# Kernel optimization log

Measured on AMD Instinct MI355X. Metric: run time of the kernel, lower is better.

Reference implementation:

```python
import jax, jax.numpy as jnp
import numpy as np

# Structural constants (CSG module-level globals)
S, N = 250, 200            # sequences, peds per sequence (uniform for vectorization)
MAX = 16                   # MAX_CONSIDERED_PED
H, E = 64, 64              # h_dim, EMBEDDING_DIM
HID, BN = 512, 32          # mlp_pre_pool hidden, BOTTLENECK_DIM


def setup_inputs() -> dict:
    key = jax.random.key(0)
    ks = jax.random.split(key, 8)
    g = lambda k, shape, s=0.05: jax.random.normal(k, shape, dtype=jnp.float32) * s
    h_states = jax.random.normal(ks[0], (S * N, H), dtype=jnp.float32)
    last_pos = jax.random.normal(ks[1], (S * N, 2), dtype=jnp.float32) * 5.0
    starts = np.arange(S, dtype=np.int64) * N
    seq_start_end = jnp.asarray(np.stack([starts, starts + N], axis=1))
    return {
        "h_states": h_states,
        "last_pos": last_pos,
        "W_pos": g(ks[2], (2, E)), "b_pos": jnp.zeros((E,), jnp.float32),
        "W1": g(ks[3], (H + E, HID)), "b1": jnp.zeros((HID,), jnp.float32),
        "W2": g(ks[4], (HID, BN)), "b2": jnp.zeros((BN,), jnp.float32),
        "W_attn": g(ks[5], (MAX * BN, MAX)), "b_attn": jnp.zeros((MAX,), jnp.float32),
        "seq_start_end": seq_start_end,
        "train_or_test": 0,
    }


def reference(h_states, last_pos, W_pos, b_pos, W1, b1, W2, b2, W_attn, b_attn,
              seq_start_end, train_or_test):
    h = h_states.reshape(S, N, H)          # per-sequence hidden states
    pos = last_pos.reshape(S, N, 2)
    # social_features[s, i, j] = pos[s, j] - pos[s, i]
    rel = pos[:, None, :, :] - pos[:, :, None, :]          # [S, N, N, 2]
    # pairwise distances only feed argsort -> stop_gradient (avoids sqrt(0) NaN in vjp)
    dist = jnp.linalg.norm(jax.lax.stop_gradient(rel), axis=-1)  # [S, N, N]
    idx = jnp.argsort(dist, axis=-1)
    # original torch code sorts rows by the attached idx-value column then truncates:
    # this selects rows j with idx[s,i,j] < MAX, i.e. the inverse permutation prefix
    sel = jnp.argsort(idx, axis=-1)[..., :MAX]             # [S, N, MAX]
    # gather neighbor hidden states and relative positions
    h_sel = jax.vmap(lambda hh, ss: hh[ss])(h, sel)        # [S, N, MAX, H]
    feat_sel = jnp.take_along_axis(rel, sel[..., None], axis=2)  # [S, N, MAX, 2]
    emb = feat_sel @ W_pos + b_pos                         # pos_embedding, [S,N,MAX,E]
    x = jnp.concatenate([h_sel, emb], axis=-1)             # [S, N, MAX, H+E]
    # mlp_pre_pool: Linear->ReLU, Linear->ReLU (batch_norm off, dropout 0)
    x = jax.nn.relu(x @ W1 + b1)                           # [S, N, MAX, HID]
    x = jax.nn.relu(x @ W2 + b2)                           # [S, N, MAX, BN]
    logits = x.reshape(S, N, MAX * BN) @ W_attn + b_attn   # [S, N, MAX]
    w = jax.nn.softmax(logits, axis=-1)
    out = jnp.sum(x * w[..., None], axis=2)                # attention-weighted pool
    return out.reshape(S * N, BN)
```

## Files before the change

kernel.cpp:

```cpp
#include <hip/hip_runtime.h>
#include <hip/hip_bf16.h>

#define S_CNT 250
#define N_PED 200
#define MAXP  16
#define HID   512
#define BN    32

#define WS1_FRAGS 8192
#define WS2_FRAGS 2048
#define WAF_FRAGS 1024
#define WS_NEED   180224u

typedef __attribute__((ext_vector_type(8))) short short8;
typedef __attribute__((ext_vector_type(4))) float floatx4;

__device__ __forceinline__ short f2bu(float f) {
    union { __hip_bfloat16 h; unsigned short u; } c;
    c.h = __float2bfloat16(f);
    return (short)c.u;
}

__global__ __launch_bounds__(256) void cvt_kernel(
    const float* __restrict__ W1, const float* __restrict__ W2,
    const float* __restrict__ Wa,
    short8* __restrict__ ws1, short8* __restrict__ ws2,
    short8* __restrict__ waf)
{
    int t = blockIdx.x * 256 + threadIdx.x;
    if (t < WS1_FRAGS) {
        int lane = t & 63, ks = (t >> 6) & 3, nt = (t >> 8) & 3, pass = t >> 10;
        int n  = pass * 64 + nt * 16 + (lane & 15);
        int k0 = ks * 32 + ((lane >> 4) << 3);
        short8 v;
#pragma unroll
        for (int j = 0; j < 8; ++j) v[j] = f2bu(W1[(k0 + j) * HID + n]);
        ws1[t] = v;
    } else if (t < WS1_FRAGS + WS2_FRAGS) {
        int t2 = t - WS1_FRAGS;
        int lane = t2 & 63, nt2 = (t2 >> 6) & 1, kcl = (t2 >> 7) & 1, pass = t2 >> 8;
        int kc = pass * 2 + kcl;
        int n  = nt2 * 16 + (lane & 15);
        int k0 = kc * 32 + ((lane >> 4) << 3);
        short8 v;
#pragma unroll
        for (int j = 0; j < 8; ++j) v[j] = f2bu(W2[(k0 + j) * BN + n]);
        ws2[t2] = v;
    } else if (t < WS1_FRAGS + WS2_FRAGS + WAF_FRAGS) {
        int t3 = t - (WS1_FRAGS + WS2_FRAGS);
        int lane = t3 & 63, kt = t3 >> 6;
        int n  = lane & 15;
        int k0 = kt * 32 + ((lane >> 4) << 3);
        short8 v;
#pragma unroll
        for (int j = 0; j < 8; ++j) v[j] = f2bu(Wa[(k0 + j) * MAXP + n]);
        waf[t3] = v;
    }
}

__global__ __launch_bounds__(256, 2) void fused_pre(
    const float* __restrict__ h_states, const float* __restrict__ last_pos,
    const float* __restrict__ Wpos,     const float* __restrict__ bpos,
    const float* __restrict__ b1,       const float* __restrict__ b2,
    const float* __restrict__ ba,
    const short8* __restrict__ ws1,     const short8* __restrict__ ws2,
    const short8* __restrict__ waf,
    float* __restrict__ out)
{
    __shared__ unsigned short X1c[4][2][16][42];
    __shared__ float X2s[4][2][512];
    __shared__ float px[N_PED], py[N_PED];
    __shared__ float WS[4][16];

    const int tid = threadIdx.x;
    const int wv  = tid >> 6;
    const int ln  = tid & 63;
    const int q8  = (ln >> 4) << 3;
    const int c15 = ln & 15;
    const int s    = blockIdx.x / 25;
    const int base = s * N_PED;
    const int il0  = (blockIdx.x % 25) * 8 + wv * 2;

    if (tid < N_PED) {
        px[tid] = last_pos[(base + tid) * 2 + 0];
        py[tid] = last_pos[(base + tid) * 2 + 1];
    }
    __syncthreads();

    short8  af[2][4];
    floatx4 c2[2][2] = {};
    for (int pedi = 0; pedi < 2; ++pedi) {
        const int il = il0 + pedi;
        const float xi = px[il], yi = py[il];
        const int mm = c15, qq = ln >> 4;
        int cnt;
        {
            float dxm = __fsub_rn(px[mm], xi), dym = __fsub_rn(py[mm], yi);
            float dm = __fsqrt_rn(__builtin_fmaf(dxm, dxm, __fmul_rn(dym, dym)));
            cnt = 0;
            for (int j = qq * 50; j < qq * 50 + 50; ++j) {
                float dx = __fsub_rn(px[j], xi), dy = __fsub_rn(py[j], yi);
                float dj = __fsqrt_rn(__builtin_fmaf(dx, dx, __fmul_rn(dy, dy)));
                cnt += (dj < dm || (dj == dm && j < mm)) ? 1 : 0;
            }
            cnt += __shfl_xor(cnt, 16, 64);
            cnt += __shfl_xor(cnt, 32, 64);
        }
        const int sm = cnt;
#pragma unroll
        for (int ks = 0; ks < 2; ++ks) {
            const float* hp = &h_states[(base + sm) * 64 + ks * 32 + q8];
            short8 v;
#pragma unroll
            for (int j = 0; j < 8; ++j) v[j] = f2bu(hp[j]);
            af[pedi][ks] = v;
        }
        const float fx = px[sm] - xi, fy = py[sm] - yi;
#pragma unroll
        for (int ks = 2; ks < 4; ++ks) {
            int e0 = (ks - 2) * 32 + q8;
            short8 v;
#pragma unroll
            for (int j = 0; j < 8; ++j) {
                float e = fx * Wpos[e0 + j] + fy * Wpos[64 + e0 + j] + bpos[e0 + j];
                v[j] = f2bu(e);
            }
            af[pedi][ks] = v;
        }
    }

    for (int p = 0; p < 8; ++p) {
#pragma unroll
        for (int ntl = 0; ntl < 4; ++ntl) {
            const int nt = p * 4 + ntl;
            short8 bf[4];
#pragma unroll
            for (int ks = 0; ks < 4; ++ks)
                bf[ks] = ws1[p * 1024 + ntl * 256 + ks * 64 + ln];
            const float bb = b1[nt * 16 + c15];
            const int colb = (ntl & 1) * 16 + c15;
#pragma unroll
            for (int pedi = 0; pedi < 2; ++pedi) {
                floatx4 c = {};
#pragma unroll
                for (int ks = 0; ks < 4; ++ks)
                    c = __builtin_amdgcn_mfma_f32_16x16x32_bf16(
                            af[pedi][ks], bf[ks], c, 0, 0, 0);
#pragma unroll
                for (int r = 0; r < 4; ++r)
                    X1c[wv][pedi][(ln >> 4) * 4 + r][colb] =
                        (unsigned short)f2bu(fmaxf(c[r] + bb, 0.f));
            }
            if (ntl & 1) {
                const int kcl = ntl >> 1;
                short8 w20 = ws2[p * 256 + kcl * 128 + ln];
                short8 w21 = ws2[p * 256 + kcl * 128 + 64 + ln];
#pragma unroll
                for (int pedi = 0; pedi < 2; ++pedi) {
                    short8 a2 = *(const short8*)&X1c[wv][pedi][c15][q8];
                    c2[pedi][0] = __builtin_amdgcn_mfma_f32_16x16x32_bf16(
                            a2, w20, c2[pedi][0], 0, 0, 0);
                    c2[pedi][1] = __builtin_amdgcn_mfma_f32_16x16x32_bf16(
                            a2, w21, c2[pedi][1], 0, 0, 0);
                }
            }
        }
    }

#pragma unroll
    for (int pedi = 0; pedi < 2; ++pedi)
#pragma unroll
        for (int nt2 = 0; nt2 < 2; ++nt2) {
            const float bb2 = b2[nt2 * 16 + c15];
#pragma unroll
            for (int r = 0; r < 4; ++r)
                X2s[wv][pedi][((ln >> 4) * 4 + r) * 32 + nt2 * 16 + c15] =
                    fmaxf(c2[pedi][nt2][r] + bb2, 0.f);
        }

    floatx4 cl;
    {
        const float bav = ba[c15];
        cl[0] = bav; cl[1] = bav; cl[2] = 0.f; cl[3] = 0.f;
    }
    const float* xbase = &X2s[wv][c15 & 1][q8];
#pragma unroll
    for (int kt = 0; kt < 16; ++kt) {
        const float* xp = xbase + kt * 32;
        short8 a;
#pragma unroll
        for (int j = 0; j < 8; ++j) a[j] = f2bu(xp[j]);
        cl = __builtin_amdgcn_mfma_f32_16x16x32_bf16(a, waf[kt * 64 + ln], cl, 0, 0, 0);
    }
    const float lg0 = __shfl(cl[0], c15, 64);
    const float lg1 = __shfl(cl[1], c15, 64);

#pragma unroll
    for (int pedi = 0; pedi < 2; ++pedi) {
        const float lgf = pedi ? lg1 : lg0;
        float mxv = lgf;
        mxv = fmaxf(mxv, __shfl_xor(mxv, 1, 64));
        mxv = fmaxf(mxv, __shfl_xor(mxv, 2, 64));
        mxv = fmaxf(mxv, __shfl_xor(mxv, 4, 64));
        mxv = fmaxf(mxv, __shfl_xor(mxv, 8, 64));
        const float ev = __expf(lgf - mxv);
        float se = ev;
        se += __shfl_xor(se, 1, 64);
        se += __shfl_xor(se, 2, 64);
        se += __shfl_xor(se, 4, 64);
        se += __shfl_xor(se, 8, 64);
        if (ln < 16) WS[wv][ln] = ev / se;
        if (ln < BN) {
            float o = 0.f;
#pragma unroll
            for (int m = 0; m < MAXP; ++m)
                o += WS[wv][m] * X2s[wv][pedi][m * BN + ln];
            out[(base + il0 + pedi) * BN + ln] = o;
        }
    }
}

__global__ __launch_bounds__(256, 2) void fused_fb(
    const float* __restrict__ h_states, const float* __restrict__ last_pos,
    const float* __restrict__ Wpos,     const float* __restrict__ bpos,
    const float* __restrict__ W1,       const float* __restrict__ b1,
    const float* __restrict__ W2,       const float* __restrict__ b2,
    const float* __restrict__ Wa,       const float* __restrict__ ba,
    float* __restrict__ out)
{
    __shared__ short8 fb1[1024];
    __shared__ short8 fb2[256];
    __shared__ unsigned short X1c[4][16][40];
    __shared__ float X2s[4][512];
    __shared__ float px[N_PED], py[N_PED];
    __shared__ float LG[4][16], WS[4][16];

    const int tid = threadIdx.x;
    const int wv  = tid >> 6;
    const int ln  = tid & 63;
    const int q8  = (ln >> 4) << 3;
    const int c15 = ln & 15;
    const int s    = blockIdx.x / 25;
    const int base = s * N_PED;
    const int il0  = (blockIdx.x % 25) * 8 + wv * 2;

    if (tid < N_PED) {
        px[tid] = last_pos[(base + tid) * 2 + 0];
        py[tid] = last_pos[(base + tid) * 2 + 1];
    }
    __syncthreads();

    short8  af[2][4];
    floatx4 c2[2][2] = {};
    for (int pedi = 0; pedi < 2; ++pedi) {
        const int il = il0 + pedi;
        const float xi = px[il], yi = py[il];
        const int mm = c15, qq = ln >> 4;
        int cnt;
        {
            float dxm = __fsub_rn(px[mm], xi), dym = __fsub_rn(py[mm], yi);
            float dm = __fsqrt_rn(__builtin_fmaf(dxm, dxm, __fmul_rn(dym, dym)));
            cnt = 0;
            for (int j = qq * 50; j < qq * 50 + 50; ++j) {
                float dx = __fsub_rn(px[j], xi), dy = __fsub_rn(py[j], yi);
                float dj = __fsqrt_rn(__builtin_fmaf(dx, dx, __fmul_rn(dy, dy)));
                cnt += (dj < dm || (dj == dm && j < mm)) ? 1 : 0;
            }
            cnt += __shfl_xor(cnt, 16, 64);
            cnt += __shfl_xor(cnt, 32, 64);
        }
        const int sm = cnt;
#pragma unroll
        for (int ks = 0; ks < 2; ++ks) {
            const float* hp = &h_states[(base + sm) * 64 + ks * 32 + q8];
            short8 v;
#pragma unroll
            for (int j = 0; j < 8; ++j) v[j] = f2bu(hp[j]);
            af[pedi][ks] = v;
        }
        const float fx = px[sm] - xi, fy = py[sm] - yi;
#pragma unroll
        for (int ks = 2; ks < 4; ++ks) {
            int e0 = (ks - 2) * 32 + q8;
            short8 v;
#pragma unroll
            for (int j = 0; j < 8; ++j) {
                float e = fx * Wpos[e0 + j] + fy * Wpos[64 + e0 + j] + bpos[e0 + j];
                v[j] = f2bu(e);
            }
            af[pedi][ks] = v;
        }
    }

    for (int p = 0; p < 8; ++p) {
        __syncthreads();
        for (int f = tid; f < 1024; f += 256) {
            int lane = f & 63, ks = (f >> 6) & 3, nt = f >> 8;
            int n  = p * 64 + nt * 16 + (lane & 15);
            int k0 = ks * 32 + ((lane >> 4) << 3);
            short8 v;
#pragma unroll
            for (int j = 0; j < 8; ++j) v[j] = f2bu(W1[(k0 + j) * HID + n]);
            fb1[f] = v;
        }
        {
            int lane = tid & 63, nt2 = (tid >> 6) & 1, kcl = tid >> 7;
            int kc = p * 2 + kcl;
            int n  = nt2 * 16 + (lane & 15);
            int k0 = kc * 32 + ((lane >> 4) << 3);
            short8 v;
#pragma unroll
            for (int j = 0; j < 8; ++j) v[j] = f2bu(W2[(k0 + j) * BN + n]);
            fb2[tid] = v;
        }
        __syncthreads();
#pragma unroll
        for (int pedi = 0; pedi < 2; ++pedi) {
#pragma unroll
            for (int ntl = 0; ntl < 4; ++ntl) {
                const int nt = p * 4 + ntl;
                floatx4 c = {};
#pragma unroll
                for (int ks = 0; ks < 4; ++ks)
                    c = __builtin_amdgcn_mfma_f32_16x16x32_bf16(
                            af[pedi][ks], fb1[ntl * 256 + ks * 64 + ln], c, 0, 0, 0);
                const float bb = b1[nt * 16 + c15];
                const int colb = (ntl & 1) * 16 + c15;
#pragma unroll
                for (int r = 0; r < 4; ++r)
                    X1c[wv][(ln >> 4) * 4 + r][colb] =
                        (unsigned short)f2bu(fmaxf(c[r] + bb, 0.f));
                if (ntl & 1) {
                    const int kcl = ntl >> 1;
                    short8 a2 = *(const short8*)&X1c[wv][c15][q8];
                    c2[pedi][0] = __builtin_amdgcn_mfma_f32_16x16x32_bf16(
                            a2, fb2[kcl * 128 + ln], c2[pedi][0], 0, 0, 0);
                    c2[pedi][1] = __builtin_amdgcn_mfma_f32_16x16x32_bf16(
                            a2, fb2[kcl * 128 + 64 + ln], c2[pedi][1], 0, 0, 0);
                }
            }
        }
    }

    for (int pedi = 0; pedi < 2; ++pedi) {
#pragma unroll
        for (int nt2 = 0; nt2 < 2; ++nt2) {
            const float bb2 = b2[nt2 * 16 + c15];
#pragma unroll
            for (int r = 0; r < 4; ++r)
                X2s[wv][((ln >> 4) * 4 + r) * 32 + nt2 * 16 + c15] =
                    fmaxf(c2[pedi][nt2][r] + bb2, 0.f);
        }
        {
            int t = c15, g = ln >> 4;
            float lg = 0.f;
            for (int k = g * 128; k < g * 128 + 128; ++k)
                lg += X2s[wv][k] * Wa[k * MAXP + t];
            lg += __shfl_xor(lg, 16, 64);
            lg += __shfl_xor(lg, 32, 64);
            if (ln < 16) LG[wv][ln] = lg + ba[ln];
        }
        float mx = -1e30f;
#pragma unroll
        for (int m = 0; m < MAXP; ++m) mx = fmaxf(mx, LG[wv][m]);
        float sum = 0.f;
#pragma unroll
        for (int m = 0; m < MAXP; ++m) sum += expf(LG[wv][m] - mx);
        if (ln < 16) WS[wv][ln] = expf(LG[wv][ln] - mx) / sum;
        if (ln < BN) {
            float o = 0.f;
#pragma unroll
            for (int m = 0; m < MAXP; ++m) o += WS[wv][m] * X2s[wv][m * BN + ln];
            out[(base + il0 + pedi) * BN + ln] = o;
        }
    }
}

extern "C" void kernel_launch(void* const* d_in, const int* in_sizes, int n_in,
                              void* d_out, int out_size, void* d_ws, size_t ws_size,
                              hipStream_t stream) {
    const float* h_states = (const float*)d_in[0];
    const float* last_pos = (const float*)d_in[1];
    const float* Wpos     = (const float*)d_in[2];
    const float* bpos     = (const float*)d_in[3];
    const float* W1       = (const float*)d_in[4];
    const float* b1       = (const float*)d_in[5];
    const float* W2       = (const float*)d_in[6];
    const float* b2       = (const float*)d_in[7];
    const float* Wa       = (const float*)d_in[8];
    const float* ba       = (const float*)d_in[9];

    short8* ws1 = (short8*)d_ws;
    short8* ws2 = ws1 + WS1_FRAGS;
    short8* waf = ws2 + WS2_FRAGS;
    const int grid = (S_CNT * N_PED) / 8;

    if (ws_size >= WS_NEED) {
        cvt_kernel<<<44, 256, 0, stream>>>(W1, W2, Wa, ws1, ws2, waf);
        fused_pre<<<grid, 256, 0, stream>>>(
            h_states, last_pos, Wpos, bpos, b1, b2, ba, ws1, ws2, waf, (float*)d_out);
    } else {
        fused_fb<<<grid, 256, 0, stream>>>(
            h_states, last_pos, Wpos, bpos, W1, b1, W2, b2, Wa, ba, (float*)d_out);
    }
}
```

Before: 290.1 us.

## Stage W1 fragments through double-buffered shared memory shared by all waves

Each block now cooperatively loads W1 bf16 fragments into a two-slot shared-memory ring, prefetching the next half-panel into registers while the current one feeds the MFMAs. Previously each of the four waves read the same fragments from global memory on its own. The per-wave X1c and X2s scratch now alias one union buffer so the extra LDS fits. The cost is a block-wide barrier in each of the 16 steps, which ties the four waves together, plus extra registers for the staged loads.

```diff
diff --git a/kernel.cpp b/kernel.cpp
--- a/kernel.cpp
+++ b/kernel.cpp
@@ -67,8 +67,8 @@
     const short8* __restrict__ waf,
     float* __restrict__ out)
 {
-    __shared__ unsigned short X1c[4][2][16][42];
-    __shared__ float X2s[4][2][512];
+    __shared__ short8 sws1[2][512];
+    __shared__ __align__(16) unsigned char ubuf[4][4096];
     __shared__ float px[N_PED], py[N_PED];
     __shared__ float WS[4][16];
 
@@ -81,11 +81,20 @@
     const int base = s * N_PED;
     const int il0  = (blockIdx.x % 25) * 8 + wv * 2;
 
+    unsigned short (*X1c)[16][40] =
+        reinterpret_cast<unsigned short (*)[16][40]>(ubuf[wv]);
+    float (*X2s)[512] =
+        reinterpret_cast<float (*)[512]>(ubuf[wv]);
+
     if (tid < N_PED) {
         px[tid] = last_pos[(base + tid) * 2 + 0];
         py[tid] = last_pos[(base + tid) * 2 + 1];
     }
+    short8 st0a = ws1[tid];
+    short8 st0b = ws1[256 + tid];
     __syncthreads();
+    sws1[0][tid]       = st0a;
+    sws1[0][256 + tid] = st0b;
 
     short8  af[2][4];
     floatx4 c2[2][2] = {};
@@ -128,15 +137,30 @@
             af[pedi][ks] = v;
         }
     }
-
-    for (int p = 0; p < 8; ++p) {
-#pragma unroll
-        for (int ntl = 0; ntl < 4; ++ntl) {
-            const int nt = p * 4 + ntl;
+    __syncthreads();
+
+    for (int hp = 0; hp < 16; ++hp) {
+        const int rb = hp & 1;
+        const int p  = hp >> 1;
+        const int kcl = hp & 1;
+        short8 stga, stgb;
+        if (hp < 15) {
+            const short8* src = ws1 + (hp + 1) * 512;
+            stga = src[tid];
+            stgb = src[256 + tid];
+        }
+        short8 w20 = ws2[p * 256 + kcl * 128 + ln];
+        short8 w21 = ws2[p * 256 + kcl * 128 + 64 + ln];
+
+        const short8* cur = sws1[rb];
+#pragma unroll
+        for (int l = 0; l < 2; ++l) {
+            const int ntl = rb * 2 + l;
+            const int nt  = p * 4 + ntl;
             short8 bf[4];
 #pragma unroll
             for (int ks = 0; ks < 4; ++ks)
-                bf[ks] = ws1[p * 1024 + ntl * 256 + ks * 64 + ln];
+                bf[ks] = cur[l * 256 + ks * 64 + ln];
             const float bb = b1[nt * 16 + c15];
             const int colb = (ntl & 1) * 16 + c15;
 #pragma unroll
@@ -148,16 +172,13 @@
                             af[pedi][ks], bf[ks], c, 0, 0, 0);
 #pragma unroll
                 for (int r = 0; r < 4; ++r)
-                    X1c[wv][pedi][(ln >> 4) * 4 + r][colb] =
+                    X1c[pedi][(ln >> 4) * 4 + r][colb] =
                         (unsigned short)f2bu(fmaxf(c[r] + bb, 0.f));
             }
-            if (ntl & 1) {
-                const int kcl = ntl >> 1;
-                short8 w20 = ws2[p * 256 + kcl * 128 + ln];
-                short8 w21 = ws2[p * 256 + kcl * 128 + 64 + ln];
+            if (l == 1) {
 #pragma unroll
                 for (int pedi = 0; pedi < 2; ++pedi) {
-                    short8 a2 = *(const short8*)&X1c[wv][pedi][c15][q8];
+                    short8 a2 = *(const short8*)&X1c[pedi][c15][q8];
                     c2[pedi][0] = __builtin_amdgcn_mfma_f32_16x16x32_bf16(
                             a2, w20, c2[pedi][0], 0, 0, 0);
                     c2[pedi][1] = __builtin_amdgcn_mfma_f32_16x16x32_bf16(
@@ -165,6 +186,12 @@
                 }
             }
         }
+        if (hp < 15) {
+            short8* dstb = sws1[rb ^ 1];
+            dstb[tid]       = stga;
+            dstb[256 + tid] = stgb;
+            __syncthreads();
+        }
     }
 
 #pragma unroll
@@ -174,7 +201,7 @@
             const float bb2 = b2[nt2 * 16 + c15];
 #pragma unroll
             for (int r = 0; r < 4; ++r)
-                X2s[wv][pedi][((ln >> 4) * 4 + r) * 32 + nt2 * 16 + c15] =
+                X2s[pedi][((ln >> 4) * 4 + r) * 32 + nt2 * 16 + c15] =
                     fmaxf(c2[pedi][nt2][r] + bb2, 0.f);
         }
 
@@ -183,7 +210,7 @@
         const float bav = ba[c15];
         cl[0] = bav; cl[1] = bav; cl[2] = 0.f; cl[3] = 0.f;
     }
-    const float* xbase = &X2s[wv][c15 & 1][q8];
+    const float* xbase = &X2s[c15 & 1][q8];
 #pragma unroll
     for (int kt = 0; kt < 16; ++kt) {
         const float* xp = xbase + kt * 32;
@@ -214,7 +241,7 @@
             float o = 0.f;
 #pragma unroll
             for (int m = 0; m < MAXP; ++m)
-                o += WS[wv][m] * X2s[wv][pedi][m * BN + ln];
+                o += WS[wv][m] * X2s[pedi][m * BN + ln];
             out[(base + il0 + pedi) * BN + ln] = o;
         }
     }
```

After: 301.2 us. +3.8%, slower.

## Pass layer-1 MFMA outputs to layer-2 via lane shuffles instead of LDS

Applied to the files above, without the earlier changes.

Swaps the MFMA operand order for the first layer so each lane holds a transposed output tile. The ReLU'd results are packed to bf16 pairs and moved into the layer-2 A-operand layout with cross-lane shuffles, which removes the X1c shared-memory staging buffer and its scattered 16-bit stores. Biases now load as vectors. The distance-rank comparison is also folded into a single 64-bit key compare. This aims to cut LDS traffic and latency in the MLP inner loop, at the cost of eight ds_bpermute shuffles plus selects per pedestrian tile.

```diff
diff --git a/kernel.cpp b/kernel.cpp
--- a/kernel.cpp
+++ b/kernel.cpp
@@ -19,6 +19,12 @@
     union { __hip_bfloat16 h; unsigned short u; } c;
     c.h = __float2bfloat16(f);
     return (short)c.u;
+}
+
+__device__ __forceinline__ unsigned int pk2(float lo, float hi) {
+    union { __hip_bfloat162 h; unsigned int u; } c;
+    c.h = __float22bfloat162_rn(float2{lo, hi});
+    return c.u;
 }
 
 __global__ __launch_bounds__(256) void cvt_kernel(
@@ -67,7 +73,6 @@
     const short8* __restrict__ waf,
     float* __restrict__ out)
 {
-    __shared__ unsigned short X1c[4][2][16][42];
     __shared__ float X2s[4][2][512];
     __shared__ float px[N_PED], py[N_PED];
     __shared__ float WS[4][16];
@@ -80,6 +85,11 @@
     const int s    = blockIdx.x / 25;
     const int base = s * N_PED;
     const int il0  = (blockIdx.x % 25) * 8 + wv * 2;
+
+    const int g    = ln >> 4;
+    const int s0i  = ((g & 1) << 5) + c15;
+    const int s1i  = s0i + 16;
+    const bool up  = (ln >= 32);
 
     if (tid < N_PED) {
         px[tid] = last_pos[(base + tid) * 2 + 0];
@@ -97,11 +107,15 @@
         {
             float dxm = __fsub_rn(px[mm], xi), dym = __fsub_rn(py[mm], yi);
             float dm = __fsqrt_rn(__builtin_fmaf(dxm, dxm, __fmul_rn(dym, dym)));
+            const unsigned long long keym =
+                (((unsigned long long)__float_as_uint(dm)) << 32) | (unsigned)mm;
             cnt = 0;
             for (int j = qq * 50; j < qq * 50 + 50; ++j) {
                 float dx = __fsub_rn(px[j], xi), dy = __fsub_rn(py[j], yi);
                 float dj = __fsqrt_rn(__builtin_fmaf(dx, dx, __fmul_rn(dy, dy)));
-                cnt += (dj < dm || (dj == dm && j < mm)) ? 1 : 0;
+                const unsigned long long keyj =
+                    (((unsigned long long)__float_as_uint(dj)) << 32) | (unsigned)j;
+                cnt += (keyj < keym) ? 1 : 0;
             }
             cnt += __shfl_xor(cnt, 16, 64);
             cnt += __shfl_xor(cnt, 32, 64);
@@ -131,38 +145,54 @@
 
     for (int p = 0; p < 8; ++p) {
 #pragma unroll
-        for (int ntl = 0; ntl < 4; ++ntl) {
-            const int nt = p * 4 + ntl;
-            short8 bf[4];
-#pragma unroll
-            for (int ks = 0; ks < 4; ++ks)
-                bf[ks] = ws1[p * 1024 + ntl * 256 + ks * 64 + ln];
-            const float bb = b1[nt * 16 + c15];
-            const int colb = (ntl & 1) * 16 + c15;
+        for (int kcl = 0; kcl < 2; ++kcl) {
+            short8 w20 = ws2[p * 256 + kcl * 128 + ln];
+            short8 w21 = ws2[p * 256 + kcl * 128 + 64 + ln];
+            floatx4 cc[2][2] = {};
+#pragma unroll
+            for (int h = 0; h < 2; ++h) {
+                const int ntl = kcl * 2 + h;
+                short8 bf[4];
+#pragma unroll
+                for (int ks = 0; ks < 4; ++ks)
+                    bf[ks] = ws1[p * 1024 + ntl * 256 + ks * 64 + ln];
+#pragma unroll
+                for (int pedi = 0; pedi < 2; ++pedi)
+#pragma unroll
+                    for (int ks = 0; ks < 4; ++ks)
+                        cc[pedi][h] = __builtin_amdgcn_mfma_f32_16x16x32_bf16(
+                                bf[ks], af[pedi][ks], cc[pedi][h], 0, 0, 0);
+            }
+            const int nt0 = (p * 2 + kcl) * 2;
+            const floatx4 bbe = *(const floatx4*)&b1[nt0 * 16 + 4 * g];
+            const floatx4 bbo = *(const floatx4*)&b1[(nt0 + 1) * 16 + 4 * g];
 #pragma unroll
             for (int pedi = 0; pedi < 2; ++pedi) {
-                floatx4 c = {};
-#pragma unroll
-                for (int ks = 0; ks < 4; ++ks)
-                    c = __builtin_amdgcn_mfma_f32_16x16x32_bf16(
-                            af[pedi][ks], bf[ks], c, 0, 0, 0);
-#pragma unroll
-                for (int r = 0; r < 4; ++r)
-                    X1c[wv][pedi][(ln >> 4) * 4 + r][colb] =
-                        (unsigned short)f2bu(fmaxf(c[r] + bb, 0.f));
-            }
-            if (ntl & 1) {
-                const int kcl = ntl >> 1;
-                short8 w20 = ws2[p * 256 + kcl * 128 + ln];
-                short8 w21 = ws2[p * 256 + kcl * 128 + 64 + ln];
-#pragma unroll
-                for (int pedi = 0; pedi < 2; ++pedi) {
-                    short8 a2 = *(const short8*)&X1c[wv][pedi][c15][q8];
-                    c2[pedi][0] = __builtin_amdgcn_mfma_f32_16x16x32_bf16(
-                            a2, w20, c2[pedi][0], 0, 0, 0);
-                    c2[pedi][1] = __builtin_amdgcn_mfma_f32_16x16x32_bf16(
-                            a2, w21, c2[pedi][1], 0, 0, 0);
-                }
+                const unsigned int e01 = pk2(fmaxf(cc[pedi][0][0] + bbe[0], 0.f),
+                                             fmaxf(cc[pedi][0][1] + bbe[1], 0.f));
+                const unsigned int e23 = pk2(fmaxf(cc[pedi][0][2] + bbe[2], 0.f),
+                                             fmaxf(cc[pedi][0][3] + bbe[3], 0.f));
+                const unsigned int o01 = pk2(fmaxf(cc[pedi][1][0] + bbo[0], 0.f),
+                                             fmaxf(cc[pedi][1][1] + bbo[1], 0.f));
+                const unsigned int o23 = pk2(fmaxf(cc[pedi][1][2] + bbo[2], 0.f),
+                                             fmaxf(cc[pedi][1][3] + bbo[3], 0.f));
+                const int ea0 = __shfl((int)e01, s0i, 64);
+                const int oa0 = __shfl((int)o01, s0i, 64);
+                const int ea1 = __shfl((int)e23, s0i, 64);
+                const int oa1 = __shfl((int)o23, s0i, 64);
+                const int ea2 = __shfl((int)e01, s1i, 64);
+                const int oa2 = __shfl((int)o01, s1i, 64);
+                const int ea3 = __shfl((int)e23, s1i, 64);
+                const int oa3 = __shfl((int)o23, s1i, 64);
+                union { unsigned int u[4]; short8 v; } a2u;
+                a2u.u[0] = up ? (unsigned)oa0 : (unsigned)ea0;
+                a2u.u[1] = up ? (unsigned)oa1 : (unsigned)ea1;
+                a2u.u[2] = up ? (unsigned)oa2 : (unsigned)ea2;
+                a2u.u[3] = up ? (unsigned)oa3 : (unsigned)ea3;
+                c2[pedi][0] = __builtin_amdgcn_mfma_f32_16x16x32_bf16(
+                        a2u.v, w20, c2[pedi][0], 0, 0, 0);
+                c2[pedi][1] = __builtin_amdgcn_mfma_f32_16x16x32_bf16(
+                        a2u.v, w21, c2[pedi][1], 0, 0, 0);
             }
         }
     }
```

Measured after the change: 348.4 us. 20.1% more time.
